# Performance work log

Measured on AMD Instinct MI355X. Metric: run time of the kernel, lower is better.

The kernel has to match this reference:

```python
import jax, jax.numpy as jnp
import numpy as np
import math

# Dims chosen per input_specs
B, Q, S, T = 8, 64, 64, 64          # batch, queries, stat (segment) count, tokens per segment
H, DH = 8, 64                        # heads, head dim
NH = H * DH                          # num_hiddens = 512
STAT_K, TOKEN_K = 8, 16
NEG = -1e6


def setup_inputs() -> dict:
    key = jax.random.key(0)
    ks = jax.random.split(key, 11)
    f = lambda k, sh: jax.random.normal(k, sh, dtype=jnp.float32)
    w = lambda k: f(k, (NH, NH)) * 0.05  # Linear weights stored as [in, out]
    return {
        "queries": f(ks[0], (B, Q, NH)),
        "stat_keys": f(ks[1], (B, S, NH)),
        "token_keys": f(ks[2], (B * S, T, NH)),
        "values": f(ks[3], (B * S, T, NH)),
        "stat_valid_lens": jax.random.randint(ks[4], (B,), 1, S + 1, dtype=jnp.int32),
        "Wq_stat": w(ks[5]),
        "Wq_token": w(ks[6]),
        "Wk_stat": w(ks[7]),
        "Wk_token": w(ks[8]),
        "Wv": w(ks[9]),
        "Wo": w(ks[10]),
    }


def reference(queries, stat_keys, token_keys, values, stat_valid_lens,
              Wq_stat, Wq_token, Wk_stat, Wk_token, Wv, Wo):
    scale = 1.0 / math.sqrt(DH)

    def split_heads(x):  # [b, L, H*DH] -> [b, H, L, DH]
        b, L, _ = x.shape
        return x.reshape(b, L, H, DH).transpose(0, 2, 1, 3)

    q_stat = split_heads(queries @ Wq_stat)        # [B,H,Q,DH]
    q_tok = split_heads(queries @ Wq_token)        # [B,H,Q,DH]
    k_stat = split_heads(stat_keys @ Wk_stat)      # [B,H,S,DH]
    # token_keys/values come in as [B*S, T, size]; per-head layout [B,H,S,T,DH]
    k_tok = (token_keys @ Wk_token).reshape(B, S, T, H, DH).transpose(0, 3, 1, 2, 4)
    v = (values @ Wv).reshape(B, S, T, H, DH).transpose(0, 3, 1, 2, 4)

    # --- stat-level scores, valid-length mask, top-k sparsification, softmax ---
    stat_scores = jnp.einsum('bhqd,bhsd->bhqs', q_stat, k_stat) * scale  # [B,H,Q,S]
    valid = jnp.arange(S)[None, None, None, :] < stat_valid_lens[:, None, None, None]
    stat_scores = jnp.where(valid, stat_scores, NEG)
    k1 = min(S - 1, STAT_K)
    _, top_idx = jax.lax.top_k(stat_scores, k1)                           # [B,H,Q,k1]
    keep = jax.nn.one_hot(top_idx, S, dtype=stat_scores.dtype).sum(-2) > 0  # [B,H,Q,S]
    stat_w = jax.nn.softmax(jnp.where(keep, stat_scores, NEG), axis=-1)   # [B,H,Q,S]

    # --- token-level scores. NOTE: the original code computes torch.topk but then
    # overwrites with the LAST k2 positions (token_weights[:, :, -k2:] = ...), so the
    # token top-k result is dead code; we faithfully reproduce the last-k2 masking. ---
    tok_scores = jnp.einsum('bhqd,bhstd->bhsqt', q_tok, k_tok) * scale    # [B,H,S,Q,T]
    k2 = min(T - 1, TOKEN_K)
    last_mask = jnp.arange(T) >= (T - k2)
    tok_w = jax.nn.softmax(jnp.where(last_mask, tok_scores, NEG), axis=-1)
    tok_w = tok_w.transpose(0, 1, 3, 2, 4)                                # [B,H,Q,S,T]

    # --- combine hierarchy and attend over values ---
    comb = stat_w[..., None] * tok_w                                      # [B,H,Q,S,T]
    out = jnp.einsum('bhqst,bhstd->bhqd', comb, v)                        # [B,H,Q,DH]
    out = out.transpose(0, 2, 1, 3).reshape(B, Q, NH)
    return out @ Wo
```

## Files before the change

### kernel.cpp

```cpp
#include <hip/hip_runtime.h>
#include <hip/hip_bf16.h>

#define BB 8
#define QQ 64
#define SS 64
#define TT 64
#define HH 8
#define DH 64
#define NHID 512
#define STAT_K 8
#define TOKEN_K 16

typedef short bf16x8 __attribute__((ext_vector_type(8)));
typedef float f32x4 __attribute__((ext_vector_type(4)));

__device__ inline ushort f2bf_rne(float x) {
    union { float f; unsigned u; } v; v.f = x;
    unsigned r = v.u + 0x7fff + ((v.u >> 16) & 1);
    return (ushort)(r >> 16);
}
__device__ inline float bf2f(ushort h) {
    union { unsigned u; float f; } v; v.u = ((unsigned)h) << 16;
    return v.f;
}

__global__ __launch_bounds__(256) void conv_w(
    const float* w0, const float* w1, const float* w2,
    const float* w3, const float* w4, const float* w5, ushort* wT)
{
    const int z = blockIdx.z;
    const float* srcs[6] = {w0, w1, w2, w3, w4, w5};
    const float* src = srcs[z];
    ushort* hi = wT + (size_t)z * 524288;
    ushort* lo = hi + 262144;
    __shared__ float t[32][33];
    const int c0 = blockIdx.x * 32, r0 = blockIdx.y * 32;
    const int tx = threadIdx.x & 31, ty = threadIdx.x >> 5;
    #pragma unroll
    for (int i = 0; i < 4; ++i)
        t[ty + 8 * i][tx] = src[(r0 + ty + 8 * i) * 512 + c0 + tx];
    __syncthreads();
    #pragma unroll
    for (int i = 0; i < 4; ++i) {
        float x = t[tx][ty + 8 * i];
        ushort h = f2bf_rne(x);
        int o = (c0 + ty + 8 * i) * 512 + r0 + tx;
        hi[o] = h;
        lo[o] = f2bf_rne(x - bf2f(h));
    }
}

__global__ __launch_bounds__(256) void gemm_split3(
    const float* __restrict__ queries, const float* __restrict__ stat_keys,
    const ushort* __restrict__ wT,
    float* __restrict__ q_stat, float* __restrict__ k_stat,
    float* __restrict__ q_tokf)
{
    const int z = blockIdx.z;
    const float* Afp = (z == 1) ? stat_keys : queries;
    const ushort* Bh = wT + (size_t)z * 524288;
    const ushort* Bl = Bh + 262144;
    float* C = (z == 0) ? q_stat : (z == 1) ? k_stat : q_tokf;
    const int K = 512, N = 512;

    __shared__ ushort As[2][64][40];
    __shared__ ushort Bs[2][64][40];
    const int tid = threadIdx.x;
    const int row0 = blockIdx.y * 64, col0 = blockIdx.x * 64;
    const int wave = tid >> 6, lane = tid & 63;
    const int wm = wave & 1, wn = wave >> 1;
    const int m16 = lane & 15, quad = lane >> 4;
    const int srow = tid >> 2, schunk = tid & 3;

    const float*  aptr  = Afp + (size_t)(row0 + srow) * K + schunk * 8;
    const ushort* bptrh = Bh + (size_t)(col0 + srow) * K + schunk * 8;
    const ushort* bptrl = Bl + (size_t)(col0 + srow) * K + schunk * 8;

    f32x4 acc[2][2];
    #pragma unroll
    for (int i = 0; i < 2; ++i)
        #pragma unroll
        for (int j = 0; j < 2; ++j)
            #pragma unroll
            for (int r = 0; r < 4; ++r) acc[i][j][r] = 0.f;

    for (int k0 = 0; k0 < K; k0 += 32) {
        float4 ax0 = ((const float4*)(aptr + k0))[0];
        float4 ax1 = ((const float4*)(aptr + k0))[1];
        uint4  bvh = *(const uint4*)(bptrh + k0);
        uint4  bvl = *(const uint4*)(bptrl + k0);
        ushort4 h0, h1, l0, l1;
        h0.x = f2bf_rne(ax0.x); l0.x = f2bf_rne(ax0.x - bf2f(h0.x));
        h0.y = f2bf_rne(ax0.y); l0.y = f2bf_rne(ax0.y - bf2f(h0.y));
        h0.z = f2bf_rne(ax0.z); l0.z = f2bf_rne(ax0.z - bf2f(h0.z));
        h0.w = f2bf_rne(ax0.w); l0.w = f2bf_rne(ax0.w - bf2f(h0.w));
        h1.x = f2bf_rne(ax1.x); l1.x = f2bf_rne(ax1.x - bf2f(h1.x));
        h1.y = f2bf_rne(ax1.y); l1.y = f2bf_rne(ax1.y - bf2f(h1.y));
        h1.z = f2bf_rne(ax1.z); l1.z = f2bf_rne(ax1.z - bf2f(h1.z));
        h1.w = f2bf_rne(ax1.w); l1.w = f2bf_rne(ax1.w - bf2f(h1.w));
        *(ushort4*)&As[0][srow][schunk * 8]     = h0;
        *(ushort4*)&As[0][srow][schunk * 8 + 4] = h1;
        *(ushort4*)&As[1][srow][schunk * 8]     = l0;
        *(ushort4*)&As[1][srow][schunk * 8 + 4] = l1;
        *(uint4*)&Bs[0][srow][schunk * 8] = bvh;
        *(uint4*)&Bs[1][srow][schunk * 8] = bvl;
        __syncthreads();

        bf16x8 af[2], bf[2], afl[2], bfl[2];
        #pragma unroll
        for (int i = 0; i < 2; ++i) {
            af[i]  = *(const bf16x8*)&As[0][wm * 32 + i * 16 + m16][quad * 8];
            bf[i]  = *(const bf16x8*)&Bs[0][wn * 32 + i * 16 + m16][quad * 8];
            afl[i] = *(const bf16x8*)&As[1][wm * 32 + i * 16 + m16][quad * 8];
            bfl[i] = *(const bf16x8*)&Bs[1][wn * 32 + i * 16 + m16][quad * 8];
        }
        #pragma unroll
        for (int i = 0; i < 2; ++i)
            #pragma unroll
            for (int j = 0; j < 2; ++j) {
                acc[i][j] = __builtin_amdgcn_mfma_f32_16x16x32_bf16(af[i], bf[j], acc[i][j], 0, 0, 0);
                acc[i][j] = __builtin_amdgcn_mfma_f32_16x16x32_bf16(af[i], bfl[j], acc[i][j], 0, 0, 0);
                acc[i][j] = __builtin_amdgcn_mfma_f32_16x16x32_bf16(afl[i], bf[j], acc[i][j], 0, 0, 0);
            }
        __syncthreads();
    }

    #pragma unroll
    for (int i = 0; i < 2; ++i)
        #pragma unroll
        for (int j = 0; j < 2; ++j) {
            int r0 = row0 + wm * 32 + i * 16 + quad * 4;
            int c = col0 + wn * 32 + j * 16 + m16;
            #pragma unroll
            for (int reg = 0; reg < 4; ++reg)
                C[(size_t)(r0 + reg) * N + c] = acc[i][j][reg];
        }
}

__global__ __launch_bounds__(256) void gemm_out(
    const ushort* __restrict__ Ah, const ushort* __restrict__ Al,
    const ushort* __restrict__ Bh, const ushort* __restrict__ Bl,
    float* __restrict__ C)
{
    const int K = 512, N = 512;
    __shared__ ushort As[2][64][40];
    __shared__ ushort Bs[2][64][40];
    const int tid = threadIdx.x;
    const int row0 = blockIdx.y * 64, col0 = blockIdx.x * 64;
    const int wave = tid >> 6, lane = tid & 63;
    const int wm = wave & 1, wn = wave >> 1;
    const int m16 = lane & 15, quad = lane >> 4;
    const int srow = tid >> 2, schunk = tid & 3;

    f32x4 acc[2][2];
    #pragma unroll
    for (int i = 0; i < 2; ++i)
        #pragma unroll
        for (int j = 0; j < 2; ++j)
            #pragma unroll
            for (int r = 0; r < 4; ++r) acc[i][j][r] = 0.f;

    for (int k0 = 0; k0 < K; k0 += 32) {
        const size_t aoff = (size_t)(row0 + srow) * K + k0 + schunk * 8;
        const size_t boff = (size_t)(col0 + srow) * K + k0 + schunk * 8;
        *(uint4*)&As[0][srow][schunk * 8] = *(const uint4*)(Ah + aoff);
        *(uint4*)&Bs[0][srow][schunk * 8] = *(const uint4*)(Bh + boff);
        *(uint4*)&As[1][srow][schunk * 8] = *(const uint4*)(Al + aoff);
        *(uint4*)&Bs[1][srow][schunk * 8] = *(const uint4*)(Bl + boff);
        __syncthreads();

        bf16x8 af[2], bf[2], afl[2], bfl[2];
        #pragma unroll
        for (int i = 0; i < 2; ++i) {
            af[i]  = *(const bf16x8*)&As[0][wm * 32 + i * 16 + m16][quad * 8];
            bf[i]  = *(const bf16x8*)&Bs[0][wn * 32 + i * 16 + m16][quad * 8];
            afl[i] = *(const bf16x8*)&As[1][wm * 32 + i * 16 + m16][quad * 8];
            bfl[i] = *(const bf16x8*)&Bs[1][wn * 32 + i * 16 + m16][quad * 8];
        }
        #pragma unroll
        for (int i = 0; i < 2; ++i)
            #pragma unroll
            for (int j = 0; j < 2; ++j) {
                acc[i][j] = __builtin_amdgcn_mfma_f32_16x16x32_bf16(af[i], bf[j], acc[i][j], 0, 0, 0);
                acc[i][j] = __builtin_amdgcn_mfma_f32_16x16x32_bf16(af[i], bfl[j], acc[i][j], 0, 0, 0);
                acc[i][j] = __builtin_amdgcn_mfma_f32_16x16x32_bf16(afl[i], bf[j], acc[i][j], 0, 0, 0);
            }
        __syncthreads();
    }

    #pragma unroll
    for (int i = 0; i < 2; ++i)
        #pragma unroll
        for (int j = 0; j < 2; ++j) {
            int r0 = row0 + wm * 32 + i * 16 + quad * 4;
            int c = col0 + wn * 32 + j * 16 + m16;
            #pragma unroll
            for (int reg = 0; reg < 4; ++reg)
                C[(size_t)(r0 + reg) * N + c] = acc[i][j][reg];
        }
}

__global__ __launch_bounds__(256) void gemm_tok(
    const float* __restrict__ token_keys, const float* __restrict__ values,
    const ushort* __restrict__ wkt_h, const ushort* __restrict__ wv_h,
    ushort* __restrict__ k_tok, ushort* __restrict__ v_proj)
{
    const int z = blockIdx.z;
    const float* A = z ? values : token_keys;
    const ushort* Bh = z ? wv_h : wkt_h;
    ushort* C = z ? v_proj : k_tok;
    const int K = 512, N = 512;

    __shared__ ushort As[64][40];
    __shared__ ushort Bs[256][40];
    const int tid = threadIdx.x;
    const int row0 = blockIdx.y * 64, col0 = blockIdx.x * 256;
    const int wave = tid >> 6, lane = tid & 63;
    const int m16 = lane & 15, quad = lane >> 4;
    const int srow = tid >> 2, schunk = tid & 3;

    const int r = row0 + srow;
    const size_t arow = (size_t)((r >> 4) * 64 + 48 + (r & 15)) * K;

    f32x4 acc[4][4];
    #pragma unroll
    for (int i = 0; i < 4; ++i)
        #pragma unroll
        for (int j = 0; j < 4; ++j)
            #pragma unroll
            for (int rr = 0; rr < 4; ++rr) acc[i][j][rr] = 0.f;

    for (int k0 = 0; k0 < K; k0 += 32) {
        const float* ap = A + arow + k0 + schunk * 8;
        float4 x0 = ((const float4*)ap)[0];
        float4 x1 = ((const float4*)ap)[1];
        ushort4 h0, h1;
        h0.x = f2bf_rne(x0.x); h0.y = f2bf_rne(x0.y);
        h0.z = f2bf_rne(x0.z); h0.w = f2bf_rne(x0.w);
        h1.x = f2bf_rne(x1.x); h1.y = f2bf_rne(x1.y);
        h1.z = f2bf_rne(x1.z); h1.w = f2bf_rne(x1.w);
        *(ushort4*)&As[srow][schunk * 8] = h0;
        *(ushort4*)&As[srow][schunk * 8 + 4] = h1;
        #pragma unroll
        for (int i = 0; i < 4; ++i) {
            int v = tid + i * 256;
            int brow = v >> 2, bchunk = v & 3;
            *(uint4*)&Bs[brow][bchunk * 8] =
                *(const uint4*)(Bh + (size_t)(col0 + brow) * K + k0 + bchunk * 8);
        }
        __syncthreads();

        bf16x8 af[4], bf[4];
        #pragma unroll
        for (int i = 0; i < 4; ++i) {
            af[i] = *(const bf16x8*)&As[i * 16 + m16][quad * 8];
            bf[i] = *(const bf16x8*)&Bs[wave * 64 + i * 16 + m16][quad * 8];
        }
        #pragma unroll
        for (int i = 0; i < 4; ++i)
            #pragma unroll
            for (int j = 0; j < 4; ++j)
                acc[i][j] = __builtin_amdgcn_mfma_f32_16x16x32_bf16(af[i], bf[j], acc[i][j], 0, 0, 0);
        __syncthreads();
    }

    #pragma unroll
    for (int i = 0; i < 4; ++i)
        #pragma unroll
        for (int j = 0; j < 4; ++j) {
            int r0 = row0 + i * 16 + quad * 4;
            int c = col0 + wave * 64 + j * 16 + m16;
            #pragma unroll
            for (int reg = 0; reg < 4; ++reg)
                C[(size_t)(r0 + reg) * N + c] = f2bf_rne(acc[i][j][reg]);
        }
}

__global__ __launch_bounds__(64) void attend_fused(
    const float* __restrict__ q_stat, const float* __restrict__ k_stat,
    const float* __restrict__ q_tok, const ushort* __restrict__ k_tok,
    const ushort* __restrict__ v_proj, const int* __restrict__ valid_lens,
    ushort* __restrict__ ctx_hi, ushort* __restrict__ ctx_lo)
{
    const int bid = blockIdx.x;
    const int b = bid >> 9, h = (bid >> 6) & 7, q = bid & 63;
    const int lane = threadIdx.x;

    __shared__ float sq[64];
    __shared__ float ssc[16];

    sq[lane] = q_stat[(b * QQ + q) * NHID + h * DH + lane];
    __syncthreads();

    const float4* kr = (const float4*)(k_stat + (b * SS + lane) * NHID + h * DH);
    const float4* sq4 = (const float4*)sq;
    float sc = 0.f;
    #pragma unroll
    for (int i = 0; i < 16; ++i) {
        float4 a = sq4[i], kk = kr[i];
        sc += a.x * kk.x + a.y * kk.y + a.z * kk.z + a.w * kk.w;
    }
    sc *= 0.125f;
    if (lane >= valid_lens[b]) sc = -1e6f;

    float my = sc;
    float mv[STAT_K]; int mi[STAT_K];
    #pragma unroll
    for (int j = 0; j < STAT_K; ++j) {
        float v = my; int idx = lane;
        #pragma unroll
        for (int off = 32; off > 0; off >>= 1) {
            float ov = __shfl_down(v, off);
            int   oi = __shfl_down(idx, off);
            if (ov > v || (ov == v && oi < idx)) { v = ov; idx = oi; }
        }
        v = __shfl(v, 0); idx = __shfl(idx, 0);
        mv[j] = v; mi[j] = idx;
        if (lane == idx) my = -3e38f;
    }
    float m0 = mv[0], den = 0.f, w[STAT_K];
    #pragma unroll
    for (int j = 0; j < STAT_K; ++j) { w[j] = __expf(mv[j] - m0); den += w[j]; }
    float inv = 1.f / den;

    __syncthreads();
    sq[lane] = q_tok[(size_t)(b * QQ + q) * NHID + h * DH + lane];
    __syncthreads();

    const int t = lane >> 2, part = lane & 3;
    float acc = 0.f;

    #pragma unroll
    for (int j = 0; j < STAT_K; ++j) {
        const int s = mi[j];
        const float wseg = w[j] * inv;
        const size_t rowbase = (size_t)((b * SS + s) * TOKEN_K);

        const uint4* k4 = (const uint4*)(k_tok + (rowbase + t) * NHID + h * DH + part * 16);
        uint4 ka = k4[0], kb = k4[1];
        const float* qb = &sq[part * 16];
        float p = 0.f;
        p += qb[0]  * bf2f((ushort)(ka.x & 0xffff)) + qb[1]  * bf2f((ushort)(ka.x >> 16));
        p += qb[2]  * bf2f((ushort)(ka.y & 0xffff)) + qb[3]  * bf2f((ushort)(ka.y >> 16));
        p += qb[4]  * bf2f((ushort)(ka.z & 0xffff)) + qb[5]  * bf2f((ushort)(ka.z >> 16));
        p += qb[6]  * bf2f((ushort)(ka.w & 0xffff)) + qb[7]  * bf2f((ushort)(ka.w >> 16));
        p += qb[8]  * bf2f((ushort)(kb.x & 0xffff)) + qb[9]  * bf2f((ushort)(kb.x >> 16));
        p += qb[10] * bf2f((ushort)(kb.y & 0xffff)) + qb[11] * bf2f((ushort)(kb.y >> 16));
        p += qb[12] * bf2f((ushort)(kb.z & 0xffff)) + qb[13] * bf2f((ushort)(kb.z >> 16));
        p += qb[14] * bf2f((ushort)(kb.w & 0xffff)) + qb[15] * bf2f((ushort)(kb.w >> 16));
        p += __shfl_xor(p, 1);
        p += __shfl_xor(p, 2);
        if (part == 0) ssc[t] = p * 0.125f;
        __syncthreads();

        float m = ssc[0];
        #pragma unroll
        for (int tt = 1; tt < TOKEN_K; ++tt) m = fmaxf(m, ssc[tt]);
        float dent = 0.f, wv[TOKEN_K];
        #pragma unroll
        for (int tt = 0; tt < TOKEN_K; ++tt) { wv[tt] = __expf(ssc[tt] - m); dent += wv[tt]; }

        const ushort* vrow = v_proj + rowbase * NHID + h * DH + lane;
        float loc = 0.f;
        #pragma unroll
        for (int tt = 0; tt < TOKEN_K; ++tt) loc += wv[tt] * bf2f(vrow[tt * NHID]);
        acc += (wseg / dent) * loc;
        __syncthreads();
    }

    const size_t o = (size_t)(b * QQ + q) * NHID + h * DH + lane;
    ushort hh = f2bf_rne(acc);
    ctx_hi[o] = hh;
    ctx_lo[o] = f2bf_rne(acc - bf2f(hh));
}

extern "C" void kernel_launch(void* const* d_in, const int* in_sizes, int n_in,
                              void* d_out, int out_size, void* d_ws, size_t ws_size,
                              hipStream_t stream) {
    const float* queries    = (const float*)d_in[0];
    const float* stat_keys  = (const float*)d_in[1];
    const float* token_keys = (const float*)d_in[2];
    const float* values     = (const float*)d_in[3];
    const int*   valid_lens = (const int*)d_in[4];
    const float* Wq_stat    = (const float*)d_in[5];
    const float* Wq_token   = (const float*)d_in[6];
    const float* Wk_stat    = (const float*)d_in[7];
    const float* Wk_token   = (const float*)d_in[8];
    const float* Wv         = (const float*)d_in[9];
    const float* Wo         = (const float*)d_in[10];

    char* w = (char*)d_ws;
    ushort* wT      = (ushort*)(w + 0);
    float*  q_stat  = (float*)(w + 6291456);
    float*  k_stat  = (float*)(w + 7340032);
    float*  q_tokf  = (float*)(w + 8388608);
    ushort* k_tok   = (ushort*)(w + 9437184);
    ushort* v_projp = (ushort*)(w + 17825792);
    ushort* ctx_hi  = (ushort*)(w + 26214400);
    ushort* ctx_lo  = ctx_hi + 262144;

    ushort* wkt_h = wT + 3 * 524288;
    ushort* wv_h  = wT + 4 * 524288;
    ushort* wo_h  = wT + 5 * 524288, *wo_l = wo_h + 262144;

    conv_w<<<dim3(16, 16, 6), 256, 0, stream>>>(
        Wq_stat, Wk_stat, Wq_token, Wk_token, Wv, Wo, wT);

    gemm_split3<<<dim3(8, 8, 3), 256, 0, stream>>>(
        queries, stat_keys, wT, q_stat, k_stat, q_tokf);

    gemm_tok<<<dim3(2, 128, 2), 256, 0, stream>>>(
        token_keys, values, wkt_h, wv_h, k_tok, v_projp);

    attend_fused<<<4096, 64, 0, stream>>>(
        q_stat, k_stat, q_tokf, k_tok, v_projp, valid_lens, ctx_hi, ctx_lo);

    gemm_out<<<dim3(8, 8), 256, 0, stream>>>(
        ctx_hi, ctx_lo, wo_h, wo_l, (float*)d_out);
}
```

Measured before the change: 251.9 us.

## Rewrite attention as dense MFMA over all segments with transposed V projection

```diff
diff --git a/kernel.cpp b/kernel.cpp
--- a/kernel.cpp
+++ b/kernel.cpp
@@ -201,16 +201,10 @@
 }
 
 __global__ __launch_bounds__(256) void gemm_tok(
-    const float* __restrict__ token_keys, const float* __restrict__ values,
-    const ushort* __restrict__ wkt_h, const ushort* __restrict__ wv_h,
-    ushort* __restrict__ k_tok, ushort* __restrict__ v_proj)
+    const float* __restrict__ token_keys, const ushort* __restrict__ wkt_h,
+    ushort* __restrict__ k_tok)
 {
-    const int z = blockIdx.z;
-    const float* A = z ? values : token_keys;
-    const ushort* Bh = z ? wv_h : wkt_h;
-    ushort* C = z ? v_proj : k_tok;
     const int K = 512, N = 512;
-
     __shared__ ushort As[64][40];
     __shared__ ushort Bs[256][40];
     const int tid = threadIdx.x;
@@ -231,7 +225,7 @@
             for (int rr = 0; rr < 4; ++rr) acc[i][j][rr] = 0.f;
 
     for (int k0 = 0; k0 < K; k0 += 32) {
-        const float* ap = A + arow + k0 + schunk * 8;
+        const float* ap = token_keys + arow + k0 + schunk * 8;
         float4 x0 = ((const float4*)ap)[0];
         float4 x1 = ((const float4*)ap)[1];
         ushort4 h0, h1;
@@ -246,7 +240,7 @@
             int v = tid + i * 256;
             int brow = v >> 2, bchunk = v & 3;
             *(uint4*)&Bs[brow][bchunk * 8] =
-                *(const uint4*)(Bh + (size_t)(col0 + brow) * K + k0 + bchunk * 8);
+                *(const uint4*)(wkt_h + (size_t)(col0 + brow) * K + k0 + bchunk * 8);
         }
         __syncthreads();
 
@@ -272,106 +266,239 @@
             int c = col0 + wave * 64 + j * 16 + m16;
             #pragma unroll
             for (int reg = 0; reg < 4; ++reg)
-                C[(size_t)(r0 + reg) * N + c] = f2bf_rne(acc[i][j][reg]);
-        }
-}
-
-__global__ __launch_bounds__(64) void attend_fused(
+                k_tok[(size_t)(r0 + reg) * N + c] = f2bf_rne(acc[i][j][reg]);
+        }
+}
+
+__global__ __launch_bounds__(256) void gemm_vT(
+    const float* __restrict__ values, const ushort* __restrict__ wv_h,
+    ushort* __restrict__ vT)
+{
+    const int K = 512;
+    __shared__ ushort As[256][40];
+    __shared__ ushort Bs[64][40];
+    const int tid = threadIdx.x;
+    const int row0m = blockIdx.y * 256, col0n = blockIdx.x * 64;
+    const int wave = tid >> 6, lane = tid & 63;
+    const int m16 = lane & 15, quad = lane >> 4;
+    const int srow = tid >> 2, schunk = tid & 3;
+
+    const int n = col0n + srow;
+    const size_t brow = (size_t)((n >> 4) * 64 + 48 + (n & 15)) * K;
+
+    f32x4 acc[4][4];
+    #pragma unroll
+    for (int i = 0; i < 4; ++i)
+        #pragma unroll
+        for (int j = 0; j < 4; ++j)
+            #pragma unroll
+            for (int rr = 0; rr < 4; ++rr) acc[i][j][rr] = 0.f;
+
+    for (int k0 = 0; k0 < K; k0 += 32) {
+        const float* bp = values + brow + k0 + schunk * 8;
+        float4 x0 = ((const float4*)bp)[0];
+        float4 x1 = ((const float4*)bp)[1];
+        ushort4 h0, h1;
+        h0.x = f2bf_rne(x0.x); h0.y = f2bf_rne(x0.y);
+        h0.z = f2bf_rne(x0.z); h0.w = f2bf_rne(x0.w);
+        h1.x = f2bf_rne(x1.x); h1.y = f2bf_rne(x1.y);
+        h1.z = f2bf_rne(x1.z); h1.w = f2bf_rne(x1.w);
+        *(ushort4*)&Bs[srow][schunk * 8] = h0;
+        *(ushort4*)&Bs[srow][schunk * 8 + 4] = h1;
+        #pragma unroll
+        for (int i = 0; i < 4; ++i) {
+            int v = tid + i * 256;
+            int ar = v >> 2, ac = v & 3;
+            *(uint4*)&As[ar][ac * 8] =
+                *(const uint4*)(wv_h + (size_t)(row0m + ar) * K + k0 + ac * 8);
+        }
+        __syncthreads();
+
+        bf16x8 af[4], bf[4];
+        #pragma unroll
+        for (int i = 0; i < 4; ++i) {
+            af[i] = *(const bf16x8*)&As[wave * 64 + i * 16 + m16][quad * 8];
+            bf[i] = *(const bf16x8*)&Bs[i * 16 + m16][quad * 8];
+        }
+        #pragma unroll
+        for (int i = 0; i < 4; ++i)
+            #pragma unroll
+            for (int j = 0; j < 4; ++j)
+                acc[i][j] = __builtin_amdgcn_mfma_f32_16x16x32_bf16(af[i], bf[j], acc[i][j], 0, 0, 0);
+        __syncthreads();
+    }
+
+    #pragma unroll
+    for (int i = 0; i < 4; ++i)
+        #pragma unroll
+        for (int j = 0; j < 4; ++j) {
+            int m = row0m + wave * 64 + i * 16 + quad * 4;
+            int c = col0n + j * 16 + m16;
+            #pragma unroll
+            for (int reg = 0; reg < 4; ++reg)
+                vT[(size_t)(m + reg) * 8192 + c] = f2bf_rne(acc[i][j][reg]);
+        }
+}
+
+__global__ __launch_bounds__(256) void attend_mfma(
     const float* __restrict__ q_stat, const float* __restrict__ k_stat,
-    const float* __restrict__ q_tok, const ushort* __restrict__ k_tok,
-    const ushort* __restrict__ v_proj, const int* __restrict__ valid_lens,
+    const float* __restrict__ q_tokf, const ushort* __restrict__ k_tok,
+    const ushort* __restrict__ vT, const int* __restrict__ valid_lens,
     ushort* __restrict__ ctx_hi, ushort* __restrict__ ctx_lo)
 {
-    const int bid = blockIdx.x;
-    const int b = bid >> 9, h = (bid >> 6) & 7, q = bid & 63;
-    const int lane = threadIdx.x;
-
-    __shared__ float sq[64];
-    __shared__ float ssc[16];
-
-    sq[lane] = q_stat[(b * QQ + q) * NHID + h * DH + lane];
+    const int wg = blockIdx.x;
+    const int b = wg >> 5, h = (wg >> 2) & 7, qt = wg & 3;
+    const int tid = threadIdx.x, wave = tid >> 6, lane = tid & 63;
+    const int m16 = lane & 15, quad = lane >> 4;
+
+    __shared__ float  sQs[16][64];
+    __shared__ ushort sQt[2][16][72];
+    __shared__ float  sW[16][64];
+    __shared__ ushort sKt[128][72];
+    __shared__ ushort sCb[2][16][520];
+
+    {
+        int row = tid >> 4, c4 = tid & 15;
+        const size_t qrow = (size_t)(b * 64 + qt * 16 + row) * 512 + h * 64;
+        float4 xs = *(const float4*)(q_stat + qrow + c4 * 4);
+        *(float4*)&sQs[row][c4 * 4] = xs;
+        float4 xt = *(const float4*)(q_tokf + qrow + c4 * 4);
+        ushort4 hh, ll;
+        hh.x = f2bf_rne(xt.x); ll.x = f2bf_rne(xt.x - bf2f(hh.x));
+        hh.y = f2bf_rne(xt.y); ll.y = f2bf_rne(xt.y - bf2f(hh.y));
+        hh.z = f2bf_rne(xt.z); ll.z = f2bf_rne(xt.z - bf2f(hh.z));
+        hh.w = f2bf_rne(xt.w); ll.w = f2bf_rne(xt.w - bf2f(hh.w));
+        *(ushort4*)&sQt[0][row][c4 * 4] = hh;
+        *(ushort4*)&sQt[1][row][c4 * 4] = ll;
+    }
     __syncthreads();
 
-    const float4* kr = (const float4*)(k_stat + (b * SS + lane) * NHID + h * DH);
-    const float4* sq4 = (const float4*)sq;
-    float sc = 0.f;
-    #pragma unroll
-    for (int i = 0; i < 16; ++i) {
-        float4 a = sq4[i], kk = kr[i];
-        sc += a.x * kk.x + a.y * kk.y + a.z * kk.z + a.w * kk.w;
-    }
-    sc *= 0.125f;
-    if (lane >= valid_lens[b]) sc = -1e6f;
-
-    float my = sc;
-    float mv[STAT_K]; int mi[STAT_K];
-    #pragma unroll
-    for (int j = 0; j < STAT_K; ++j) {
-        float v = my; int idx = lane;
-        #pragma unroll
-        for (int off = 32; off > 0; off >>= 1) {
-            float ov = __shfl_down(v, off);
-            int   oi = __shfl_down(idx, off);
-            if (ov > v || (ov == v && oi < idx)) { v = ov; idx = oi; }
-        }
-        v = __shfl(v, 0); idx = __shfl(idx, 0);
-        mv[j] = v; mi[j] = idx;
-        if (lane == idx) my = -3e38f;
-    }
-    float m0 = mv[0], den = 0.f, w[STAT_K];
-    #pragma unroll
-    for (int j = 0; j < STAT_K; ++j) { w[j] = __expf(mv[j] - m0); den += w[j]; }
-    float inv = 1.f / den;
-
-    __syncthreads();
-    sq[lane] = q_tok[(size_t)(b * QQ + q) * NHID + h * DH + lane];
-    __syncthreads();
-
-    const int t = lane >> 2, part = lane & 3;
-    float acc = 0.f;
-
-    #pragma unroll
-    for (int j = 0; j < STAT_K; ++j) {
-        const int s = mi[j];
-        const float wseg = w[j] * inv;
-        const size_t rowbase = (size_t)((b * SS + s) * TOKEN_K);
-
-        const uint4* k4 = (const uint4*)(k_tok + (rowbase + t) * NHID + h * DH + part * 16);
-        uint4 ka = k4[0], kb = k4[1];
-        const float* qb = &sq[part * 16];
-        float p = 0.f;
-        p += qb[0]  * bf2f((ushort)(ka.x & 0xffff)) + qb[1]  * bf2f((ushort)(ka.x >> 16));
-        p += qb[2]  * bf2f((ushort)(ka.y & 0xffff)) + qb[3]  * bf2f((ushort)(ka.y >> 16));
-        p += qb[4]  * bf2f((ushort)(ka.z & 0xffff)) + qb[5]  * bf2f((ushort)(ka.z >> 16));
-        p += qb[6]  * bf2f((ushort)(ka.w & 0xffff)) + qb[7]  * bf2f((ushort)(ka.w >> 16));
-        p += qb[8]  * bf2f((ushort)(kb.x & 0xffff)) + qb[9]  * bf2f((ushort)(kb.x >> 16));
-        p += qb[10] * bf2f((ushort)(kb.y & 0xffff)) + qb[11] * bf2f((ushort)(kb.y >> 16));
-        p += qb[12] * bf2f((ushort)(kb.z & 0xffff)) + qb[13] * bf2f((ushort)(kb.z >> 16));
-        p += qb[14] * bf2f((ushort)(kb.w & 0xffff)) + qb[15] * bf2f((ushort)(kb.w >> 16));
-        p += __shfl_xor(p, 1);
-        p += __shfl_xor(p, 2);
-        if (part == 0) ssc[t] = p * 0.125f;
-        __syncthreads();
-
-        float m = ssc[0];
-        #pragma unroll
-        for (int tt = 1; tt < TOKEN_K; ++tt) m = fmaxf(m, ssc[tt]);
-        float dent = 0.f, wv[TOKEN_K];
-        #pragma unroll
-        for (int tt = 0; tt < TOKEN_K; ++tt) { wv[tt] = __expf(ssc[tt] - m); dent += wv[tt]; }
-
-        const ushort* vrow = v_proj + rowbase * NHID + h * DH + lane;
-        float loc = 0.f;
-        #pragma unroll
-        for (int tt = 0; tt < TOKEN_K; ++tt) loc += wv[tt] * bf2f(vrow[tt * NHID]);
-        acc += (wseg / dent) * loc;
-        __syncthreads();
-    }
-
-    const size_t o = (size_t)(b * QQ + q) * NHID + h * DH + lane;
-    ushort hh = f2bf_rne(acc);
-    ctx_hi[o] = hh;
-    ctx_lo[o] = f2bf_rne(acc - bf2f(hh));
+    bf16x8 aQh[2], aQl[2];
+    #pragma unroll
+    for (int ks = 0; ks < 2; ++ks) {
+        aQh[ks] = *(const bf16x8*)&sQt[0][m16][ks * 32 + quad * 8];
+        aQl[ks] = *(const bf16x8*)&sQt[1][m16][ks * 32 + quad * 8];
+    }
+
+    const int vlen = valid_lens[b];
+    for (int qq = 0; qq < 4; ++qq) {
+        const int q = wave * 4 + qq;
+        const float4* kr = (const float4*)(k_stat + (size_t)(b * SS + lane) * NHID + h * DH);
+        const float4* sq4 = (const float4*)&sQs[q][0];
+        float sc = 0.f;
+        #pragma unroll
+        for (int i = 0; i < 16; ++i) {
+            float4 a = sq4[i], kk = kr[i];
+            sc += a.x * kk.x + a.y * kk.y + a.z * kk.z + a.w * kk.w;
+        }
+        sc *= 0.125f;
+        if (lane >= vlen) sc = -1e6f;
+
+        float my = sc;
+        float mv[STAT_K]; int mi[STAT_K];
+        #pragma unroll
+        for (int j = 0; j < STAT_K; ++j) {
+            float v = my; int idx = lane;
+            #pragma unroll
+            for (int off = 32; off > 0; off >>= 1) {
+                float ov = __shfl_down(v, off);
+                int   oi = __shfl_down(idx, off);
+                if (ov > v || (ov == v && oi < idx)) { v = ov; idx = oi; }
+            }
+            v = __shfl(v, 0); idx = __shfl(idx, 0);
+            mv[j] = v; mi[j] = idx;
+            if (lane == idx) my = -3e38f;
+        }
+        float m0 = mv[0], den = 0.f, w[STAT_K];
+        #pragma unroll
+        for (int j = 0; j < STAT_K; ++j) { w[j] = __expf(mv[j] - m0); den += w[j]; }
+        float inv = 1.f / den;
+        float wl = 0.f;
+        #pragma unroll
+        for (int j = 0; j < STAT_K; ++j)
+            if (lane == mi[j]) wl = w[j] * inv;
+        sW[q][lane] = wl;
+    }
+
+    f32x4 oacc;
+    #pragma unroll
+    for (int r = 0; r < 4; ++r) oacc[r] = 0.f;
+
+    const ushort* vrow = vT + (size_t)(h * 64 + wave * 16 + m16) * 8192
+                            + (size_t)b * 1024 + quad * 8;
+
+    for (int half = 0; half < 2; ++half) {
+        for (int g = 0; g < 4; ++g) {
+            __syncthreads();
+            {
+                const ushort* base = k_tok
+                    + (size_t)(b * 1024 + half * 512 + g * 128) * 512 + h * 64;
+                #pragma unroll
+                for (int i = 0; i < 4; ++i) {
+                    int idx = i * 256 + tid;
+                    int row = idx >> 3, ch = idx & 7;
+                    *(uint4*)&sKt[row][ch * 8] =
+                        *(const uint4*)(base + (size_t)row * 512 + ch * 8);
+                }
+            }
+            __syncthreads();
+
+            #pragma unroll
+            for (int ti = 0; ti < 2; ++ti) {
+                const int sl = wave * 2 + ti;
+                const int sg = half * 32 + g * 8 + sl;
+                bf16x8 b0 = *(const bf16x8*)&sKt[sl * 16 + m16][quad * 8];
+                bf16x8 b1 = *(const bf16x8*)&sKt[sl * 16 + m16][32 + quad * 8];
+                f32x4 c;
+                #pragma unroll
+                for (int r = 0; r < 4; ++r) c[r] = 0.f;
+                c = __builtin_amdgcn_mfma_f32_16x16x32_bf16(aQh[0], b0, c, 0, 0, 0);
+                c = __builtin_amdgcn_mfma_f32_16x16x32_bf16(aQl[0], b0, c, 0, 0, 0);
+                c = __builtin_amdgcn_mfma_f32_16x16x32_bf16(aQh[1], b1, c, 0, 0, 0);
+                c = __builtin_amdgcn_mfma_f32_16x16x32_bf16(aQl[1], b1, c, 0, 0, 0);
+
+                const int klb = (g * 8 + sl) * 16 + m16;
+                #pragma unroll
+                for (int r = 0; r < 4; ++r) {
+                    float v = c[r] * 0.125f;
+                    float m = v;
+                    m = fmaxf(m, __shfl_xor(m, 1));
+                    m = fmaxf(m, __shfl_xor(m, 2));
+                    m = fmaxf(m, __shfl_xor(m, 4));
+                    m = fmaxf(m, __shfl_xor(m, 8));
+                    float e = __expf(v - m);
+                    float s = e;
+                    s += __shfl_xor(s, 1);
+                    s += __shfl_xor(s, 2);
+                    s += __shfl_xor(s, 4);
+                    s += __shfl_xor(s, 8);
+                    float wt = (e / s) * sW[quad * 4 + r][sg];
+                    ushort ch = f2bf_rne(wt);
+                    sCb[0][quad * 4 + r][klb] = ch;
+                    sCb[1][quad * 4 + r][klb] = f2bf_rne(wt - bf2f(ch));
+                }
+            }
+        }
+        __syncthreads();
+
+        #pragma unroll
+        for (int ks = 0; ks < 16; ++ks) {
+            bf16x8 bv = *(const bf16x8*)(vrow + half * 512 + ks * 32);
+            bf16x8 ah = *(const bf16x8*)&sCb[0][m16][ks * 32 + quad * 8];
+            bf16x8 al = *(const bf16x8*)&sCb[1][m16][ks * 32 + quad * 8];
+            oacc = __builtin_amdgcn_mfma_f32_16x16x32_bf16(ah, bv, oacc, 0, 0, 0);
+            oacc = __builtin_amdgcn_mfma_f32_16x16x32_bf16(al, bv, oacc, 0, 0, 0);
+        }
+    }
+
+    #pragma unroll
+    for (int r = 0; r < 4; ++r) {
+        const size_t o = (size_t)(b * 64 + qt * 16 + quad * 4 + r) * 512
+                       + h * 64 + wave * 16 + m16;
+        ushort hh = f2bf_rne(oacc[r]);
+        ctx_hi[o] = hh;
+        ctx_lo[o] = f2bf_rne(oacc[r] - bf2f(hh));
+    }
 }
 
 extern "C" void kernel_launch(void* const* d_in, const int* in_sizes, int n_in,
@@ -395,7 +522,7 @@
     float*  k_stat  = (float*)(w + 7340032);
     float*  q_tokf  = (float*)(w + 8388608);
     ushort* k_tok   = (ushort*)(w + 9437184);
-    ushort* v_projp = (ushort*)(w + 17825792);
+    ushort* vT      = (ushort*)(w + 17825792);
     ushort* ctx_hi  = (ushort*)(w + 26214400);
     ushort* ctx_lo  = ctx_hi + 262144;
 
@@ -409,11 +536,12 @@
     gemm_split3<<<dim3(8, 8, 3), 256, 0, stream>>>(
         queries, stat_keys, wT, q_stat, k_stat, q_tokf);
 
-    gemm_tok<<<dim3(2, 128, 2), 256, 0, stream>>>(
-        token_keys, values, wkt_h, wv_h, k_tok, v_projp);
-
-    attend_fused<<<4096, 64, 0, stream>>>(
-        q_stat, k_stat, q_tokf, k_tok, v_projp, valid_lens, ctx_hi, ctx_lo);
+    gemm_tok<<<dim3(2, 128), 256, 0, stream>>>(token_keys, wkt_h, k_tok);
+
+    gemm_vT<<<dim3(128, 2), 256, 0, stream>>>(values, wv_h, vT);
+
+    attend_mfma<<<256, 256, 0, stream>>>(
+        q_stat, k_stat, q_tokf, k_tok, vT, valid_lens, ctx_hi, ctx_lo);
 
     gemm_out<<<dim3(8, 8), 256, 0, stream>>>(
         ctx_hi, ctx_lo, wo_h, wo_l, (float*)d_out);
```

Measured after the change: 262.1 us. 1.04x slower.
